# Kernel tuning notes

Hardware: AMD Instinct MI355X
Metric: run time of the kernel (lower is better)

Reference implementation:

```python
import jax, jax.numpy as jnp
import numpy as np

B, SQ, SK, HID, NH = 4, 2048, 2048, 1024, 16
HD = HID // NH  # head dim = 64


def setup_inputs() -> dict:
    key = jax.random.key(0)
    ks = jax.random.split(key, 8)
    s = 1.0 / np.sqrt(HID)
    return {
        "hidden_states": jax.random.normal(ks[0], (B, SQ, HID), jnp.float32),
        "context": jax.random.normal(ks[1], (B, SK, HID), jnp.float32),
        "Wq": jax.random.normal(ks[2], (HID, HID), jnp.float32) * s,
        "bq": jnp.zeros((HID,), jnp.float32),
        "Wk": jax.random.normal(ks[3], (HID, HID), jnp.float32) * s,
        "bk": jnp.zeros((HID,), jnp.float32),
        "Wv": jax.random.normal(ks[4], (HID, HID), jnp.float32) * s,
        "bv": jnp.zeros((HID,), jnp.float32),
    }


def _heads(x):
    # [B, S, HID] -> [B, NH, S, HD]
    b, s, _ = x.shape
    return x.reshape(b, s, NH, HD).transpose(0, 2, 1, 3)


def reference(hidden_states, context, Wq, bq, Wk, bk, Wv, bv):
    q = _heads(hidden_states @ Wq + bq)   # [B,NH,SQ,HD]
    k = _heads(context @ Wk + bk)         # [B,NH,SK,HD]
    v = _heads(context @ Wv + bv)         # [B,NH,SK,HD]
    scores = jnp.einsum("bhqd,bhkd->bhqk", q, k) / jnp.sqrt(jnp.float32(HD))
    probs = jax.nn.softmax(scores, axis=-1)  # dropout p=0 (eval) -> identity
    ctx = jnp.einsum("bhqk,bhkd->bhqd", probs, v)
    return ctx.transpose(0, 2, 1, 3).reshape(hidden_states.shape[0], -1, NH * HD)
```

## Files before the change

### kernel.cpp

```cpp
#include <hip/hip_runtime.h>
#include <hip/hip_bf16.h>
#include <math.h>

#define DI __device__ __forceinline__

typedef unsigned short u16;
typedef unsigned int u32;
typedef __bf16 bf16x8 __attribute__((ext_vector_type(8)));
typedef float f32x4 __attribute__((ext_vector_type(4)));
typedef float f32x16 __attribute__((ext_vector_type(16)));
typedef u16 u16x4 __attribute__((ext_vector_type(4)));
typedef u16 u16x8 __attribute__((ext_vector_type(8)));
typedef u32 u32x4 __attribute__((ext_vector_type(4)));

DI void gload16(const void* g, void* l) {
  __builtin_amdgcn_global_load_lds(
      (__attribute__((address_space(1))) void*)(g),
      (__attribute__((address_space(3))) void*)(l), 16, 0, 0);
}

DI u16 f2bf(float f) {
  u32 u = __builtin_bit_cast(u32, f);
  return (u16)((u + 0x7fffu + ((u >> 16) & 1u)) >> 16);
}

DI u32 cvtpk(float lo, float hi_) {
  u32 r; asm("v_cvt_pk_bf16_f32 %0, %1, %2" : "=v"(r) : "v"(lo), "v"(hi_)); return r;
}

#define MFMA16(a, b, c) __builtin_amdgcn_mfma_f32_16x16x32_bf16(a, b, c, 0, 0, 0)
#define MFMA32(a, b, c) __builtin_amdgcn_mfma_f32_32x32x16_bf16(a, b, c, 0, 0, 0)

__global__ __launch_bounds__(256) void k_convert(const float* __restrict__ a,
                                                 const float* __restrict__ b,
                                                 u16* __restrict__ oa, u16* __restrict__ ob) {
  const float* src = blockIdx.y ? b : a;
  u16* dst = blockIdx.y ? ob : oa;
  const int n4 = (4 * 2048 * 1024) / 4;
  for (int i = blockIdx.x * blockDim.x + threadIdx.x; i < n4; i += gridDim.x * blockDim.x) {
    float4 v = ((const float4*)src)[i];
    u16x4 o;
    o[0] = f2bf(v.x); o[1] = f2bf(v.y); o[2] = f2bf(v.z); o[3] = f2bf(v.w);
    *(u16x4*)(dst + 4 * (size_t)i) = o;
  }
}

__global__ __launch_bounds__(256) void k_transW(const float* __restrict__ Wq,
                                                const float* __restrict__ Wk,
                                                const float* __restrict__ Wv,
                                                u16* __restrict__ Wt) {
  __shared__ u16 tile[64][72];
  const float* W = blockIdx.z == 0 ? Wq : (blockIdx.z == 1 ? Wk : Wv);
  u16* out = Wt + (size_t)blockIdx.z * (1024 * 1024);
  int k0 = blockIdx.x * 64, n0 = blockIdx.y * 64;
  int t = threadIdx.x, r = t >> 2, c0 = (t & 3) * 16;
  const float4* src = (const float4*)(W + (size_t)(k0 + r) * 1024 + n0 + c0);
#pragma unroll
  for (int i = 0; i < 4; ++i) {
    float4 v = src[i];
    tile[r][c0 + 4 * i + 0] = f2bf(v.x); tile[r][c0 + 4 * i + 1] = f2bf(v.y);
    tile[r][c0 + 4 * i + 2] = f2bf(v.z); tile[r][c0 + 4 * i + 3] = f2bf(v.w);
  }
  __syncthreads();
  u16x8 o0, o1;
#pragma unroll
  for (int i = 0; i < 8; ++i) { o0[i] = tile[c0 + i][r]; o1[i] = tile[c0 + 8 + i][r]; }
  u16* dst = out + (size_t)(n0 + r) * 1024 + k0 + c0;
  *(u16x8*)dst = o0; *(u16x8*)(dst + 8) = o1;
}

__global__ __launch_bounds__(256) void k_gemm(const u16* __restrict__ A,
                                              const u16* __restrict__ Bt,
                                              const float* __restrict__ bias,
                                              u16* __restrict__ C, float scale, int vt) {
  __shared__ __attribute__((aligned(16))) u16 As[2][128 * 32];
  __shared__ __attribute__((aligned(16))) u16 Bs[2][128 * 32];
  const int t = threadIdx.x, w = t >> 6, l = t & 63, g = l >> 4, lid = l & 15;
  const int wr = w >> 1, wc = w & 1;
  const int m0 = blockIdx.x * 128, n0 = blockIdx.y * 128;
  f32x4 acc[4][4] = {};

  auto stage = [&](int buf, int kt) {
    for (int i = 0; i < 2; ++i) {
      int slot = i * 256 + t;
      int row = slot >> 2, c = slot & 3;
      gload16(A + (size_t)(m0 + row) * 1024 + kt * 32 + ((c ^ (row & 3)) << 3),
              &As[buf][slot << 3]);
      gload16(Bt + (size_t)(n0 + row) * 1024 + kt * 32 + ((c ^ (row & 3)) << 3),
              &Bs[buf][slot << 3]);
    }
  };

  stage(0, 0);
  __syncthreads();
  int cur = 0;
  for (int kt = 0; kt < 32; ++kt) {
    if (kt + 1 < 32) stage(cur ^ 1, kt + 1);
    bf16x8 af[4], bfr[4];
#pragma unroll
    for (int mi = 0; mi < 4; ++mi) {
      int row = wr * 64 + mi * 16 + lid;
      af[mi] = *(const bf16x8*)&As[cur][(row << 5) + ((g ^ (row & 3)) << 3)];
    }
#pragma unroll
    for (int ni = 0; ni < 4; ++ni) {
      int row = wc * 64 + ni * 16 + lid;
      bfr[ni] = *(const bf16x8*)&Bs[cur][(row << 5) + ((g ^ (row & 3)) << 3)];
    }
#pragma unroll
    for (int mi = 0; mi < 4; ++mi)
#pragma unroll
      for (int ni = 0; ni < 4; ++ni)
        acc[mi][ni] = MFMA16(af[mi], bfr[ni], acc[mi][ni]);
    __syncthreads();
    cur ^= 1;
  }
#pragma unroll
  for (int ni = 0; ni < 4; ++ni) {
    int n = n0 + wc * 64 + ni * 16 + lid;
    float bb = bias[n];
    int h = n >> 6, d = n & 63;
#pragma unroll
    for (int mi = 0; mi < 4; ++mi) {
      int mb = m0 + wr * 64 + mi * 16 + g * 4;
      if (vt) {
        int b = mb >> 11, sl = mb & 2047;
        u16x4 o;
#pragma unroll
        for (int j = 0; j < 4; ++j) o[j] = f2bf((acc[mi][ni][j] + bb) * scale);
        *(u16x4*)&C[(size_t)(b * 16 + h) * 131072 + (size_t)d * 2048 + sl] = o;
      } else {
#pragma unroll
        for (int j = 0; j < 4; ++j) {
          int m = mb + j;
          int b = m >> 11, s = m & 2047;
          C[((size_t)(b * 16 + h) << 17) + ((size_t)s << 6) + d] =
              f2bf((acc[mi][ni][j] + bb) * scale);
        }
      }
    }
  }
}

__global__ __launch_bounds__(256) void k_attn(const u16* __restrict__ Q,
                                              const u16* __restrict__ K,
                                              const u16* __restrict__ Vt,
                                              float* __restrict__ Out) {
  __shared__ __attribute__((aligned(16))) u16 smem[16384];
  u16* Ks = smem;
  u16* Vs = smem + 8192;
  const int t = threadIdx.x, w = t >> 6, l = t & 63;
  const int ql = l & 31, hi = l >> 5;
  const int head = blockIdx.y, q0 = blockIdx.x * 128;
  const size_t hoff = (size_t)head * 131072;
  const u16* Qh = Q + hoff + (size_t)q0 * 64;
  const u16* Kh = K + hoff;
  const u16* Vh = Vt + hoff;

  for (int i = 0; i < 4; ++i) {
    int slot = i * 256 + t, row = slot >> 3, c = slot & 7;
    gload16(Qh + (size_t)row * 64 + ((c ^ (row & 7)) << 3), &smem[slot << 3]);
  }
  __syncthreads();
  bf16x8 qf[4];
  const int qrow = w * 32 + ql;
#pragma unroll
  for (int dt = 0; dt < 4; ++dt) {
    int ch = dt * 2 + hi;
    qf[dt] = *(const bf16x8*)&smem[(qrow << 6) + ((ch ^ (qrow & 7)) << 3)];
  }
  __syncthreads();

  auto stageKV = [&](int buf, int kv0) {
    for (int i = 0; i < 2; ++i) {
      int slot = i * 256 + t, row = slot >> 3, c = slot & 7;
      gload16(Kh + (size_t)(kv0 + row) * 64 + ((c ^ (row & 7)) << 3),
              &Ks[buf * 4096 + (slot << 3)]);
      gload16(Vh + (size_t)row * 2048 + kv0 + ((c ^ (row & 7)) << 3),
              &Vs[buf * 4096 + (slot << 3)]);
    }
  };

  f32x16 ot0 = {}, ot1 = {};
  float m = -1e30f, lsum = 0.f;

  stageKV(0, 0);
  __syncthreads();
  int cur = 0;
  for (int tt = 0; tt < 32; ++tt) {
    if (tt + 1 < 32) stageKV(cur ^ 1, (tt + 1) * 64);
    const u16* Kb = &Ks[cur * 4096];
    const u16* Vb = &Vs[cur * 4096];
    f32x16 st0 = {}, st1 = {};
#pragma unroll
    for (int dt = 0; dt < 4; ++dt) {
      int ch = dt * 2 + hi;
      {
        int row = ql;
        bf16x8 kf = *(const bf16x8*)&Kb[(row << 6) + ((ch ^ (row & 7)) << 3)];
        st0 = MFMA32(kf, qf[dt], st0);
      }
      {
        int row = 32 + ql;
        bf16x8 kf = *(const bf16x8*)&Kb[(row << 6) + ((ch ^ (row & 7)) << 3)];
        st1 = MFMA32(kf, qf[dt], st1);
      }
    }
    float mx[16];
#pragma unroll
    for (int r = 0; r < 16; ++r) mx[r] = fmaxf(st0[r], st1[r]);
#pragma unroll
    for (int s = 8; s; s >>= 1)
#pragma unroll
      for (int r = 0; r < s; ++r) mx[r] = fmaxf(mx[r], mx[r + s]);
    float rm = mx[0];
    rm = fmaxf(rm, __shfl_xor(rm, 32, 64));
    if (!__all(rm <= m + 8.f)) {
      float mn = fmaxf(m, rm);
      float sc = exp2f(m - mn);
      m = mn;
#pragma unroll
      for (int r = 0; r < 16; ++r) { ot0[r] *= sc; ot1[r] *= sc; }
      lsum *= sc;
    }
#pragma unroll
    for (int r = 0; r < 16; ++r) st0[r] = exp2f(st0[r] - m);
#pragma unroll
    for (int r = 0; r < 16; ++r) st1[r] = exp2f(st1[r] - m);
    float sm[16];
#pragma unroll
    for (int r = 0; r < 16; ++r) sm[r] = st0[r] + st1[r];
#pragma unroll
    for (int s = 8; s; s >>= 1)
#pragma unroll
      for (int r = 0; r < s; ++r) sm[r] += sm[r + s];
    float rs = sm[0];
    rs += __shfl_xor(rs, 32, 64);
    lsum += rs;
#define PVCHUNK(sp, rb, c)                                                    \
    do {                                                                      \
      u32 a0 = cvtpk(sp[rb + 0], sp[rb + 1]);                                 \
      u32 a1 = cvtpk(sp[rb + 2], sp[rb + 3]);                                 \
      u32 b0 = cvtpk(sp[rb + 4], sp[rb + 5]);                                 \
      u32 b1 = cvtpk(sp[rb + 6], sp[rb + 7]);                                 \
      u32 pa0 = __shfl_xor(a0, 32, 64);                                       \
      u32 pa1 = __shfl_xor(a1, 32, 64);                                       \
      u32 pb0 = __shfl_xor(b0, 32, 64);                                       \
      u32 pb1 = __shfl_xor(b1, 32, 64);                                       \
      u32x4 pw;                                                               \
      pw[0] = hi ? pb0 : a0;                                  \
      pw[1] = hi ? pb1 : a1;                                  \
      pw[2] = hi ? b0 : pa0;                                  \
      pw[3] = hi ? b1 : pa1;                                  \
      bf16x8 pf = __builtin_bit_cast(bf16x8, pw);                             \
      {                                                                       \
        int row = ql, ch = (c) * 2 + hi;                                      \
        bf16x8 vf = *(const bf16x8*)&Vb[(row << 6) + ((ch ^ (row & 7)) << 3)];\
        ot0 = MFMA32(vf, pf, ot0);                                            \
      }                                                                       \
      {                                                                       \
        int row = 32 + ql, ch = (c) * 2 + hi;                                 \
        bf16x8 vf = *(const bf16x8*)&Vb[(row << 6) + ((ch ^ (row & 7)) << 3)];\
        ot1 = MFMA32(vf, pf, ot1);                                            \
      }                                                                       \
    } while (0)
    PVCHUNK(st0, 0, 0);
    PVCHUNK(st0, 8, 1);
    PVCHUNK(st1, 0, 2);
    PVCHUNK(st1, 8, 3);
#undef PVCHUNK
    __syncthreads();
    cur ^= 1;
  }
  const int b = head >> 4, h = head & 15;
  const int qg = q0 + w * 32 + ql;
  float inv = 1.f / lsum;
  float* op = Out + ((size_t)b * 2048 + qg) * 1024 + h * 64;
#pragma unroll
  for (int rq = 0; rq < 4; ++rq) {
    f32x4 v0, v1;
#pragma unroll
    for (int j = 0; j < 4; ++j) {
      v0[j] = ot0[rq * 4 + j] * inv;
      v1[j] = ot1[rq * 4 + j] * inv;
    }
    *(f32x4*)(op + rq * 8 + 4 * hi) = v0;
    *(f32x4*)(op + 32 + rq * 8 + 4 * hi) = v1;
  }
}

extern "C" void kernel_launch(void* const* d_in, const int* in_sizes, int n_in,
                              void* d_out, int out_size, void* d_ws, size_t ws_size,
                              hipStream_t stream) {
  const float* hs  = (const float*)d_in[0];
  const float* ctx = (const float*)d_in[1];
  const float* Wq  = (const float*)d_in[2];
  const float* bq  = (const float*)d_in[3];
  const float* Wk  = (const float*)d_in[4];
  const float* bk  = (const float*)d_in[5];
  const float* Wv  = (const float*)d_in[6];
  const float* bv  = (const float*)d_in[7];
  float* out = (float*)d_out;

  u16* hsb  = (u16*)d_ws;
  u16* ctxb = hsb + 8388608;
  u16* Wt   = ctxb + 8388608;
  u16* Qb   = Wt + 3 * 1048576;
  u16* Kb   = Qb + 8388608;
  u16* Vtb  = Kb + 8388608;

  const float CC = 0.18033688011112042f;

  k_convert<<<dim3(2048, 2), 256, 0, stream>>>(hs, ctx, hsb, ctxb);
  k_transW<<<dim3(16, 16, 3), 256, 0, stream>>>(Wq, Wk, Wv, Wt);
  k_gemm<<<dim3(64, 8), 256, 0, stream>>>(hsb, Wt, bq, Qb, CC, 0);
  k_gemm<<<dim3(64, 8), 256, 0, stream>>>(ctxb, Wt + 1048576, bk, Kb, 1.0f, 0);
  k_gemm<<<dim3(64, 8), 256, 0, stream>>>(ctxb, Wt + 2097152, bv, Vtb, 1.0f, 1);
  k_attn<<<dim3(16, 64), 256, 0, stream>>>(Qb, Kb, Vtb, out);
}
```

Before: 351.6 us.

## Batch QKV GEMMs into one launch, add MFMA priority hints and attn occupancy bound

Merges the three projection GEMM launches into a single grid with a z dimension that selects Q, K or V operands. This gives 1536 blocks at once so the GPU stays fuller and two launch gaps disappear. It also wraps the MFMA sections of the GEMM and attention kernels in s_setprio raises so matrix-core issue gets priority over other waves. It sets a minimum of 4 blocks per CU on the attention kernel, which may constrain register allocation and cause spills.

```diff
diff --git a/kernel.cpp b/kernel.cpp
--- a/kernel.cpp
+++ b/kernel.cpp
@@ -69,10 +69,22 @@
   *(u16x8*)dst = o0; *(u16x8*)(dst + 8) = o1;
 }
 
-__global__ __launch_bounds__(256) void k_gemm(const u16* __restrict__ A,
-                                              const u16* __restrict__ Bt,
-                                              const float* __restrict__ bias,
-                                              u16* __restrict__ C, float scale, int vt) {
+__global__ __launch_bounds__(256) void k_gemm(const u16* __restrict__ hsb,
+                                              const u16* __restrict__ ctxb,
+                                              const u16* __restrict__ Wt,
+                                              const float* __restrict__ bq,
+                                              const float* __restrict__ bk,
+                                              const float* __restrict__ bv,
+                                              u16* __restrict__ Qb, u16* __restrict__ Kb,
+                                              u16* __restrict__ Vtb, float CC) {
+  const int z = blockIdx.z;
+  const u16* A = z ? ctxb : hsb;
+  const u16* Bt = Wt + (size_t)z * 1048576;
+  const float* bias = z == 0 ? bq : (z == 1 ? bk : bv);
+  u16* C = z == 0 ? Qb : (z == 1 ? Kb : Vtb);
+  const float scale = z == 0 ? CC : 1.0f;
+  const int vt = (z == 2);
+
   __shared__ __attribute__((aligned(16))) u16 As[2][128 * 32];
   __shared__ __attribute__((aligned(16))) u16 Bs[2][128 * 32];
   const int t = threadIdx.x, w = t >> 6, l = t & 63, g = l >> 4, lid = l & 15;
@@ -107,11 +119,13 @@
       int row = wc * 64 + ni * 16 + lid;
       bfr[ni] = *(const bf16x8*)&Bs[cur][(row << 5) + ((g ^ (row & 3)) << 3)];
     }
+    __builtin_amdgcn_s_setprio(1);
 #pragma unroll
     for (int mi = 0; mi < 4; ++mi)
 #pragma unroll
       for (int ni = 0; ni < 4; ++ni)
         acc[mi][ni] = MFMA16(af[mi], bfr[ni], acc[mi][ni]);
+    __builtin_amdgcn_s_setprio(0);
     __syncthreads();
     cur ^= 1;
   }
@@ -142,10 +156,10 @@
   }
 }
 
-__global__ __launch_bounds__(256) void k_attn(const u16* __restrict__ Q,
-                                              const u16* __restrict__ K,
-                                              const u16* __restrict__ Vt,
-                                              float* __restrict__ Out) {
+__global__ __launch_bounds__(256, 4) void k_attn(const u16* __restrict__ Q,
+                                                 const u16* __restrict__ K,
+                                                 const u16* __restrict__ Vt,
+                                                 float* __restrict__ Out) {
   __shared__ __attribute__((aligned(16))) u16 smem[16384];
   u16* Ks = smem;
   u16* Vs = smem + 8192;
@@ -192,6 +206,7 @@
     const u16* Kb = &Ks[cur * 4096];
     const u16* Vb = &Vs[cur * 4096];
     f32x16 st0 = {}, st1 = {};
+    __builtin_amdgcn_s_setprio(1);
 #pragma unroll
     for (int dt = 0; dt < 4; ++dt) {
       int ch = dt * 2 + hi;
@@ -206,6 +221,7 @@
         st1 = MFMA32(kf, qf[dt], st1);
       }
     }
+    __builtin_amdgcn_s_setprio(0);
     float mx[16];
 #pragma unroll
     for (int r = 0; r < 16; ++r) mx[r] = fmaxf(st0[r], st1[r]);
@@ -253,6 +269,7 @@
       pw[2] = hi ? b0 : pa0;                                  \
       pw[3] = hi ? b1 : pa1;                                  \
       bf16x8 pf = __builtin_bit_cast(bf16x8, pw);                             \
+      __builtin_amdgcn_s_setprio(1);                                          \
       {                                                                       \
         int row = ql, ch = (c) * 2 + hi;                                      \
         bf16x8 vf = *(const bf16x8*)&Vb[(row << 6) + ((ch ^ (row & 7)) << 3)];\
@@ -263,6 +280,7 @@
         bf16x8 vf = *(const bf16x8*)&Vb[(row << 6) + ((ch ^ (row & 7)) << 3)];\
         ot1 = MFMA32(vf, pf, ot1);                                            \
       }                                                                       \
+      __builtin_amdgcn_s_setprio(0);                                          \
     } while (0)
     PVCHUNK(st0, 0, 0);
     PVCHUNK(st0, 8, 1);
@@ -313,8 +331,6 @@
 
   k_convert<<<dim3(2048, 2), 256, 0, stream>>>(hs, ctx, hsb, ctxb);
   k_transW<<<dim3(16, 16, 3), 256, 0, stream>>>(Wq, Wk, Wv, Wt);
-  k_gemm<<<dim3(64, 8), 256, 0, stream>>>(hsb, Wt, bq, Qb, CC, 0);
-  k_gemm<<<dim3(64, 8), 256, 0, stream>>>(ctxb, Wt + 1048576, bk, Kb, 1.0f, 0);
-  k_gemm<<<dim3(64, 8), 256, 0, stream>>>(ctxb, Wt + 2097152, bv, Vtb, 1.0f, 1);
+  k_gemm<<<dim3(64, 8, 3), 256, 0, stream>>>(hsb, ctxb, Wt, bq, bk, bv, Qb, Kb, Vtb, CC);
   k_attn<<<dim3(16, 64), 256, 0, stream>>>(Qb, Kb, Vtb, out);
 }
```

Result: faster. 324.1 us (-7.8%).
